# Performance work log

Hardware: AMD Instinct MI355X
Metric: run time of the kernel (lower is better)

The kernel has to match this reference:

```python
import jax, jax.numpy as jnp
import numpy as np

H = 512          # size_half
K = 16           # n_segments
B = 8192         # batch
WIDTH = 1.0 / K  # spline bin width


def setup_inputs() -> dict:
    key = jax.random.key(0)
    ks = jax.random.split(key, 4)
    v_in = jax.random.uniform(ks[0], (B, 2 * H), dtype=jnp.float32)  # config in [0,1]
    log_density = jax.random.normal(ks[1], (B, 1), dtype=jnp.float32)
    W1 = jax.random.normal(ks[2], (H, H), dtype=jnp.float32) * (1.0 / np.sqrt(H))
    b1 = jnp.zeros((H,), dtype=jnp.float32)
    W2 = jax.random.normal(ks[3], (H, H * K), dtype=jnp.float32) * (1.0 / np.sqrt(H))
    b2 = jnp.zeros((H * K,), dtype=jnp.float32)
    return {"v_in": v_in, "log_density": log_density, "W1": W1, "b1": b1, "W2": W2, "b2": b2}


def reference(v_in, log_density, W1, b1, W2, b2):
    # even_sites=True: passive = first half, active = second half
    v_passive = v_in[:, :H]           # [B, H]
    v_active = v_in[:, H:]            # [B, H]

    # FullyConnectedNeuralNetwork: hidden layer + final layer, tanh activation on both
    h = jnp.tanh((v_passive - 0.5) @ W1 + b1)          # [B, H]
    net = jnp.tanh(h @ W2 + b2).reshape(-1, H, K)      # [B, H, K]
    p = jax.nn.softmax(net, axis=2)                    # bin probability masses P_k

    # y-coordinates of knots: CDF of the bin masses, with leading zero
    knots_y = jnp.concatenate(
        [jnp.zeros((p.shape[0], H, 1), p.dtype), jnp.cumsum(p, axis=2)], axis=2
    )                                                  # [B, H, K+1]

    # searchsorted on uniform knots linspace(0,1,K+1), then -1, clamped
    knots_x = jnp.linspace(0.0, 1.0, K + 1, dtype=v_in.dtype)
    k = jnp.clip(jnp.searchsorted(knots_x, v_active, side="left") - 1, 0, K - 1)  # [B, H]

    p_k = jnp.take_along_axis(p, k[..., None], axis=2)[..., 0]        # [B, H]
    y_lo = jnp.take_along_axis(knots_y, k[..., None], axis=2)[..., 0]  # [B, H]

    alpha = (v_active - k.astype(v_in.dtype) * WIDTH) / WIDTH          # [B, H]
    v_out_active = y_lo + alpha * p_k

    v_out = jnp.concatenate([v_passive, v_out_active], axis=1)         # [B, 2H]
    log_density_out = log_density - jnp.sum(jnp.log(p_k), axis=1, keepdims=True)  # [B, 1]
    return v_out, log_density_out
```

## Files before the change

kernel.cpp:

```cpp
#include <hip/hip_runtime.h>
#include <hip/hip_bf16.h>

#define HH   512
#define BB   8192
#define WIDTH (1.0f/16.0f)

typedef __attribute__((ext_vector_type(8))) short  short8;
typedef __attribute__((ext_vector_type(4))) float  floatx4;

typedef const __attribute__((address_space(1))) void* gptr_t;
typedef __attribute__((address_space(3))) void*       lptr_t;

__device__ __forceinline__ void gload_lds16(const void* g, void* l) {
    __builtin_amdgcn_global_load_lds((gptr_t)g, (lptr_t)l, 16, 0, 0);
}

__device__ __forceinline__ float tanh_fast(float x) {
    float e = __expf(2.0f * x);
    return 1.0f - 2.0f * __builtin_amdgcn_rcpf(e + 1.0f);
}

__global__ void prep_all(const float* __restrict__ vin, const float* __restrict__ W1,
                         const float* __restrict__ W2, const float* __restrict__ ld,
                         float* __restrict__ vout, float* __restrict__ ldout,
                         __hip_bfloat16* __restrict__ Abf,
                         __hip_bfloat16* __restrict__ W1T,
                         __hip_bfloat16* __restrict__ W2T) {
    __shared__ __align__(16) float tile[32 * 36];
    int bid = blockIdx.x, tid = threadIdx.x;
    if (bid < 4352) {
        const float* src;  __hip_bfloat16* dst;  int cols, c0, r0;
        if (bid < 4096) { src = W2; dst = W2T; cols = 8192; c0 = (bid & 255) * 32; r0 = (bid >> 8) * 32; }
        else            { int b = bid - 4096; src = W1; dst = W1T; cols = 512; c0 = (b & 15) * 32; r0 = (b >> 4) * 32; }
        int y  = tid >> 3;
        int x0 = (tid & 7) * 4;
        float4 v = *(const float4*)(src + (size_t)(r0 + y) * cols + c0 + x0);
        *(float4*)(tile + y * 36 + x0) = v;
        __syncthreads();
        int n  = tid >> 3;
        int k4 = (tid & 7) * 4;
        union { __hip_bfloat16 h[4]; uint2 u; } o;
        o.h[0] = __float2bfloat16(tile[(k4 + 0) * 36 + n]);
        o.h[1] = __float2bfloat16(tile[(k4 + 1) * 36 + n]);
        o.h[2] = __float2bfloat16(tile[(k4 + 2) * 36 + n]);
        o.h[3] = __float2bfloat16(tile[(k4 + 3) * 36 + n]);
        *(uint2*)(dst + (size_t)(c0 + n) * 512 + r0 + k4) = o.u;
    } else {
        int b = bid - 4352;
        int i = b * 256 + tid;
        int r = i >> 6, c = i & 63;
        const float4* src = (const float4*)(vin + (size_t)r * 1024 + c * 8);
        float4 f0 = src[0], f1 = src[1];
        float4* dst = (float4*)(vout + (size_t)r * 1024 + c * 8);
        dst[0] = f0; dst[1] = f1;
        union { __hip_bfloat16 h[8]; uint4 v; } u;
        u.h[0] = __float2bfloat16(f0.x - 0.5f); u.h[1] = __float2bfloat16(f0.y - 0.5f);
        u.h[2] = __float2bfloat16(f0.z - 0.5f); u.h[3] = __float2bfloat16(f0.w - 0.5f);
        u.h[4] = __float2bfloat16(f1.x - 0.5f); u.h[5] = __float2bfloat16(f1.y - 0.5f);
        u.h[6] = __float2bfloat16(f1.z - 0.5f); u.h[7] = __float2bfloat16(f1.w - 0.5f);
        *(uint4*)(Abf + (size_t)r * 512 + c * 8) = u.v;
        if (tid < 4) { int row = b * 4 + tid; ldout[row] = ld[row]; }
    }
}

__global__ __launch_bounds__(256, 4) void gemm1_kernel(
        const __hip_bfloat16* __restrict__ Abf,
        const __hip_bfloat16* __restrict__ W1T,
        const float* __restrict__ b1,
        __hip_bfloat16* __restrict__ hM) {
    __shared__ __align__(16) char smem[32768];
    short* ldsA = (short*)smem;
    short* ldsB = (short*)(smem + 16384);
    int tid = threadIdx.x;
    int lane = tid & 63;
    int wv = tid >> 6, wr = wv >> 1, wc = wv & 1;
    int q = lane >> 4, cx = lane & 15;
    int srow = tid >> 3;
    int skw  = ((tid & 7) ^ (srow & 7)) * 8;
    int rowBase = blockIdx.y * 128;
    int colBase = blockIdx.x * 128;
    floatx4 acc[4][4] = {};

    for (int k0 = 0; k0 < HH; k0 += 64) {
        #pragma unroll
        for (int j = 0; j < 4; ++j) {
            int row = j * 32 + srow;
            unsigned loff = __builtin_amdgcn_readfirstlane((unsigned)((j * 256 + (tid & 192)) * 16));
            gload_lds16(Abf + (size_t)(rowBase + row) * HH + k0 + skw, (char*)ldsA + loff);
            gload_lds16(W1T + (size_t)(colBase + row) * HH + k0 + skw, (char*)ldsB + loff);
        }
        __syncthreads();
        #pragma unroll
        for (int s = 0; s < 2; ++s) {
            short8 a[4], b[4];
            #pragma unroll
            for (int mt = 0; mt < 4; ++mt)
                a[mt] = *(const short8*)(ldsA + (wr * 64 + mt * 16 + cx) * 64
                                              + (((s * 4 + q) ^ (cx & 7)) << 3));
            #pragma unroll
            for (int nt = 0; nt < 4; ++nt)
                b[nt] = *(const short8*)(ldsB + (wc * 64 + nt * 16 + cx) * 64
                                              + (((s * 4 + q) ^ (cx & 7)) << 3));
            #pragma unroll
            for (int mt = 0; mt < 4; ++mt)
                #pragma unroll
                for (int nt = 0; nt < 4; ++nt)
                    acc[mt][nt] = __builtin_amdgcn_mfma_f32_16x16x32_bf16(a[mt], b[nt], acc[mt][nt], 0, 0, 0);
        }
        __syncthreads();
    }

    float b1v[4];
    #pragma unroll
    for (int nt = 0; nt < 4; ++nt) b1v[nt] = b1[colBase + wc * 64 + nt * 16 + cx];
    #pragma unroll
    for (int mt = 0; mt < 4; ++mt)
        #pragma unroll
        for (int nt = 0; nt < 4; ++nt) {
            int col = colBase + wc * 64 + nt * 16 + cx;
            #pragma unroll
            for (int r = 0; r < 4; ++r) {
                int row = rowBase + wr * 64 + mt * 16 + q * 4 + r;
                hM[(size_t)row * HH + col] = __float2bfloat16(tanh_fast(acc[mt][nt][r] + b1v[nt]));
            }
        }
}

__global__ __launch_bounds__(256, 4) void gemm2_kernel(
        const __hip_bfloat16* __restrict__ hM,
        const __hip_bfloat16* __restrict__ W2T,
        const float* __restrict__ b2,
        const float* __restrict__ vin,
        float* __restrict__ vout,
        float* __restrict__ ldout) {
    __shared__ __align__(16) char smem[32768];
    short* ldsA = (short*)smem;
    short* ldsB = (short*)(smem + 16384);
    float* ldsE = (float*)smem;
    int tid = threadIdx.x;
    int lane = tid & 63;
    int wv = tid >> 6, wr = wv >> 1, wc = wv & 1;
    int q = lane >> 4, cx = lane & 15;
    int srow = tid >> 3;
    int skw  = ((tid & 7) ^ (srow & 7)) * 8;
    int bid = blockIdx.x;
    int xcd = bid & 7, w = bid >> 3;
    int by  = xcd * 8 + (w & 7);
    int bx  = w >> 3;
    int rowBase = by * 128;
    int colBase = bx * 128;
    floatx4 acc[4][4] = {};

    for (int k0 = 0; k0 < HH; k0 += 64) {
        #pragma unroll
        for (int j = 0; j < 4; ++j) {
            int row = j * 32 + srow;
            unsigned loff = __builtin_amdgcn_readfirstlane((unsigned)((j * 256 + (tid & 192)) * 16));
            gload_lds16(hM  + (size_t)(rowBase + row) * HH + k0 + skw, (char*)ldsA + loff);
            gload_lds16(W2T + (size_t)(colBase + row) * HH + k0 + skw, (char*)ldsB + loff);
        }
        __syncthreads();
        #pragma unroll
        for (int s = 0; s < 2; ++s) {
            short8 a[4], b[4];
            #pragma unroll
            for (int mt = 0; mt < 4; ++mt)
                a[mt] = *(const short8*)(ldsA + (wr * 64 + mt * 16 + cx) * 64
                                              + (((s * 4 + q) ^ (cx & 7)) << 3));
            #pragma unroll
            for (int nt = 0; nt < 4; ++nt)
                b[nt] = *(const short8*)(ldsB + (wc * 64 + nt * 16 + cx) * 64
                                              + (((s * 4 + q) ^ (cx & 7)) << 3));
            #pragma unroll
            for (int mt = 0; mt < 4; ++mt)
                #pragma unroll
                for (int nt = 0; nt < 4; ++nt)
                    acc[mt][nt] = __builtin_amdgcn_mfma_f32_16x16x32_bf16(a[mt], b[nt], acc[mt][nt], 0, 0, 0);
        }
        __syncthreads();
    }

    float b2v[4];
    #pragma unroll
    for (int nt = 0; nt < 4; ++nt) b2v[nt] = b2[colBase + wc * 64 + nt * 16 + cx];

    float* myTile = ldsE + wv * (16 * 76);
    int rowL  = lane & 15;
    int gL    = lane >> 4;
    int gAbs  = bx * 8 + wc * 4 + gL;

    #pragma unroll
    for (int mt = 0; mt < 4; ++mt) {
        #pragma unroll
        for (int nt = 0; nt < 4; ++nt)
            #pragma unroll
            for (int r = 0; r < 4; ++r)
                myTile[(q * 4 + r) * 76 + nt * 16 + cx] = acc[mt][nt][r] + b2v[nt];

        floatx4 x0 = *(const floatx4*)(myTile + rowL * 76 + gL * 16);
        floatx4 x1 = *(const floatx4*)(myTile + rowL * 76 + gL * 16 + 4);
        floatx4 x2 = *(const floatx4*)(myTile + rowL * 76 + gL * 16 + 8);
        floatx4 x3 = *(const floatx4*)(myTile + rowL * 76 + gL * 16 + 12);
        float xs[16] = { x0[0],x0[1],x0[2],x0[3], x1[0],x1[1],x1[2],x1[3],
                         x2[0],x2[1],x2[2],x2[3], x3[0],x3[1],x3[2],x3[3] };

        int row = rowBase + wr * 64 + mt * 16 + rowL;
        float v = vin[(size_t)row * 1024 + 512 + gAbs];
        int k = (int)ceilf(v * 16.0f) - 1;
        k = min(15, max(0, k));

        float s = 0.0f, csum = 0.0f, ek = 0.0f;
        #pragma unroll
        for (int j = 0; j < 16; ++j) {
            float e2 = __expf(2.0f * xs[j]);
            float t  = 1.0f - 2.0f * __builtin_amdgcn_rcpf(e2 + 1.0f);
            float e  = __expf(t);
            csum += (j < k)  ? e : 0.0f;
            ek    = (j == k) ? e : ek;
            s += e;
        }
        float rs = __builtin_amdgcn_rcpf(s);
        float pk  = ek * rs;
        float ylo = csum * rs;
        float alpha = (v - (float)k * WIDTH) * 16.0f;
        vout[(size_t)row * 1024 + 512 + gAbs] = ylo + alpha * pk;

        float logp = __logf(pk);
        logp += __shfl_xor(logp, 16, 64);
        logp += __shfl_xor(logp, 32, 64);
        if (lane < 16) atomicAdd(ldout + row, -logp);
    }
}

extern "C" void kernel_launch(void* const* d_in, const int* in_sizes, int n_in,
                              void* d_out, int out_size, void* d_ws, size_t ws_size,
                              hipStream_t stream) {
    const float* vin = (const float*)d_in[0];
    const float* ld  = (const float*)d_in[1];
    const float* W1  = (const float*)d_in[2];
    const float* b1  = (const float*)d_in[3];
    const float* W2  = (const float*)d_in[4];
    const float* b2  = (const float*)d_in[5];
    float* vout  = (float*)d_out;
    float* ldout = vout + (size_t)BB * 1024;

    char* ws = (char*)d_ws;
    __hip_bfloat16* Abf = (__hip_bfloat16*)(ws);
    __hip_bfloat16* W1T = (__hip_bfloat16*)(ws + 8388608);
    __hip_bfloat16* W2T = (__hip_bfloat16*)(ws + 8912896);
    __hip_bfloat16* hM  = (__hip_bfloat16*)(ws + 17301504);

    prep_all<<<6400, 256, 0, stream>>>(vin, W1, W2, ld, vout, ldout, Abf, W1T, W2T);
    gemm1_kernel<<<dim3(4, 64), 256, 0, stream>>>(Abf, W1T, b1, hM);
    gemm2_kernel<<<4096, 256, 0, stream>>>(hM, W2T, b2, vin, vout, ldout);
}
```

Measured before the change: 194.3 us.

## Overlap W2 transpose-convert with first GEMM in a combined kernel

```diff
diff --git a/kernel.cpp b/kernel.cpp
--- a/kernel.cpp
+++ b/kernel.cpp
@@ -20,21 +20,18 @@
     return 1.0f - 2.0f * __builtin_amdgcn_rcpf(e + 1.0f);
 }
 
-__global__ void prep_all(const float* __restrict__ vin, const float* __restrict__ W1,
-                         const float* __restrict__ W2, const float* __restrict__ ld,
-                         float* __restrict__ vout, float* __restrict__ ldout,
-                         __hip_bfloat16* __restrict__ Abf,
-                         __hip_bfloat16* __restrict__ W1T,
-                         __hip_bfloat16* __restrict__ W2T) {
+__global__ void prep_small(const float* __restrict__ vin, const float* __restrict__ W1,
+                           const float* __restrict__ ld,
+                           float* __restrict__ vout, float* __restrict__ ldout,
+                           __hip_bfloat16* __restrict__ Abf,
+                           __hip_bfloat16* __restrict__ W1T) {
     __shared__ __align__(16) float tile[32 * 36];
     int bid = blockIdx.x, tid = threadIdx.x;
-    if (bid < 4352) {
-        const float* src;  __hip_bfloat16* dst;  int cols, c0, r0;
-        if (bid < 4096) { src = W2; dst = W2T; cols = 8192; c0 = (bid & 255) * 32; r0 = (bid >> 8) * 32; }
-        else            { int b = bid - 4096; src = W1; dst = W1T; cols = 512; c0 = (b & 15) * 32; r0 = (b >> 4) * 32; }
+    if (bid < 256) {
+        int c0 = (bid & 15) * 32, r0 = (bid >> 4) * 32;
         int y  = tid >> 3;
         int x0 = (tid & 7) * 4;
-        float4 v = *(const float4*)(src + (size_t)(r0 + y) * cols + c0 + x0);
+        float4 v = *(const float4*)(W1 + (size_t)(r0 + y) * 512 + c0 + x0);
         *(float4*)(tile + y * 36 + x0) = v;
         __syncthreads();
         int n  = tid >> 3;
@@ -44,9 +41,9 @@
         o.h[1] = __float2bfloat16(tile[(k4 + 1) * 36 + n]);
         o.h[2] = __float2bfloat16(tile[(k4 + 2) * 36 + n]);
         o.h[3] = __float2bfloat16(tile[(k4 + 3) * 36 + n]);
-        *(uint2*)(dst + (size_t)(c0 + n) * 512 + r0 + k4) = o.u;
+        *(uint2*)(W1T + (size_t)(c0 + n) * 512 + r0 + k4) = o.u;
     } else {
-        int b = bid - 4352;
+        int b = bid - 256;
         int i = b * 256 + tid;
         int r = i >> 6, c = i & 63;
         const float4* src = (const float4*)(vin + (size_t)r * 1024 + c * 8);
@@ -63,22 +60,43 @@
     }
 }
 
-__global__ __launch_bounds__(256, 4) void gemm1_kernel(
+__global__ __launch_bounds__(256, 4) void mega1_kernel(
         const __hip_bfloat16* __restrict__ Abf,
         const __hip_bfloat16* __restrict__ W1T,
         const float* __restrict__ b1,
-        __hip_bfloat16* __restrict__ hM) {
+        __hip_bfloat16* __restrict__ hM,
+        const float* __restrict__ W2,
+        __hip_bfloat16* __restrict__ W2T) {
     __shared__ __align__(16) char smem[32768];
+    int bid = blockIdx.x, tid = threadIdx.x;
+    if (bid >= 256) {
+        float* tile = (float*)smem;
+        int b = bid - 256;
+        int c0 = (b & 255) * 32, r0 = (b >> 8) * 32;
+        int y  = tid >> 3;
+        int x0 = (tid & 7) * 4;
+        float4 v = *(const float4*)(W2 + (size_t)(r0 + y) * 8192 + c0 + x0);
+        *(float4*)(tile + y * 36 + x0) = v;
+        __syncthreads();
+        int n  = tid >> 3;
+        int k4 = (tid & 7) * 4;
+        union { __hip_bfloat16 h[4]; uint2 u; } o;
+        o.h[0] = __float2bfloat16(tile[(k4 + 0) * 36 + n]);
+        o.h[1] = __float2bfloat16(tile[(k4 + 1) * 36 + n]);
+        o.h[2] = __float2bfloat16(tile[(k4 + 2) * 36 + n]);
+        o.h[3] = __float2bfloat16(tile[(k4 + 3) * 36 + n]);
+        *(uint2*)(W2T + (size_t)(c0 + n) * 512 + r0 + k4) = o.u;
+        return;
+    }
     short* ldsA = (short*)smem;
     short* ldsB = (short*)(smem + 16384);
-    int tid = threadIdx.x;
     int lane = tid & 63;
     int wv = tid >> 6, wr = wv >> 1, wc = wv & 1;
     int q = lane >> 4, cx = lane & 15;
     int srow = tid >> 3;
     int skw  = ((tid & 7) ^ (srow & 7)) * 8;
-    int rowBase = blockIdx.y * 128;
-    int colBase = blockIdx.x * 128;
+    int rowBase = (bid >> 2) * 128;
+    int colBase = (bid & 3) * 128;
     floatx4 acc[4][4] = {};
 
     for (int k0 = 0; k0 < HH; k0 += 64) {
@@ -250,7 +268,7 @@
     __hip_bfloat16* W2T = (__hip_bfloat16*)(ws + 8912896);
     __hip_bfloat16* hM  = (__hip_bfloat16*)(ws + 17301504);
 
-    prep_all<<<6400, 256, 0, stream>>>(vin, W1, W2, ld, vout, ldout, Abf, W1T, W2T);
-    gemm1_kernel<<<dim3(4, 64), 256, 0, stream>>>(Abf, W1T, b1, hM);
+    prep_small<<<2304, 256, 0, stream>>>(vin, W1, ld, vout, ldout, Abf, W1T);
+    mega1_kernel<<<4352, 256, 0, stream>>>(Abf, W1T, b1, hM, W2, W2T);
     gemm2_kernel<<<4096, 256, 0, stream>>>(hM, W2T, b2, vin, vout, ldout);
 }
```

New measurement: 197.0 us. No clear change (+1.4%).

## Fuse prep and both GEMMs into one persistent kernel with grid barriers

Applied to the files above, without the earlier changes.

```diff
diff --git a/kernel.cpp b/kernel.cpp
--- a/kernel.cpp
+++ b/kernel.cpp
@@ -4,6 +4,7 @@
 #define HH   512
 #define BB   8192
 #define WIDTH (1.0f/16.0f)
+#define NBLK 1024u
 
 typedef __attribute__((ext_vector_type(8))) short  short8;
 typedef __attribute__((ext_vector_type(4))) float  floatx4;
@@ -20,215 +21,214 @@
     return 1.0f - 2.0f * __builtin_amdgcn_rcpf(e + 1.0f);
 }
 
-__global__ void prep_all(const float* __restrict__ vin, const float* __restrict__ W1,
-                         const float* __restrict__ W2, const float* __restrict__ ld,
-                         float* __restrict__ vout, float* __restrict__ ldout,
-                         __hip_bfloat16* __restrict__ Abf,
-                         __hip_bfloat16* __restrict__ W1T,
-                         __hip_bfloat16* __restrict__ W2T) {
-    __shared__ __align__(16) float tile[32 * 36];
+__device__ __forceinline__ void grid_barrier(unsigned* cnt) {
+    __syncthreads();
+    if (threadIdx.x == 0) {
+        __threadfence();
+        __hip_atomic_fetch_add(cnt, 1u, __ATOMIC_ACQ_REL, __HIP_MEMORY_SCOPE_AGENT);
+        while (__hip_atomic_load(cnt, __ATOMIC_ACQUIRE, __HIP_MEMORY_SCOPE_AGENT) < NBLK)
+            __builtin_amdgcn_s_sleep(2);
+        __threadfence();
+    }
+    __syncthreads();
+}
+
+__global__ __launch_bounds__(256, 4) void fused_kernel(
+        const float* __restrict__ vin,
+        const float* __restrict__ ld,
+        const float* __restrict__ W1,
+        const float* __restrict__ b1,
+        const float* __restrict__ W2,
+        const float* __restrict__ b2,
+        float* __restrict__ vout,
+        float* __restrict__ ldout,
+        __hip_bfloat16* __restrict__ Abf,
+        __hip_bfloat16* __restrict__ W1T,
+        __hip_bfloat16* __restrict__ W2T,
+        __hip_bfloat16* __restrict__ hM,
+        unsigned* __restrict__ cnt) {
+    __shared__ __align__(16) char smem[32768];
     int bid = blockIdx.x, tid = threadIdx.x;
-    if (bid < 4352) {
-        const float* src;  __hip_bfloat16* dst;  int cols, c0, r0;
-        if (bid < 4096) { src = W2; dst = W2T; cols = 8192; c0 = (bid & 255) * 32; r0 = (bid >> 8) * 32; }
-        else            { int b = bid - 4096; src = W1; dst = W1T; cols = 512; c0 = (b & 15) * 32; r0 = (b >> 4) * 32; }
-        int y  = tid >> 3;
-        int x0 = (tid & 7) * 4;
-        float4 v = *(const float4*)(src + (size_t)(r0 + y) * cols + c0 + x0);
-        *(float4*)(tile + y * 36 + x0) = v;
-        __syncthreads();
-        int n  = tid >> 3;
-        int k4 = (tid & 7) * 4;
-        union { __hip_bfloat16 h[4]; uint2 u; } o;
-        o.h[0] = __float2bfloat16(tile[(k4 + 0) * 36 + n]);
-        o.h[1] = __float2bfloat16(tile[(k4 + 1) * 36 + n]);
-        o.h[2] = __float2bfloat16(tile[(k4 + 2) * 36 + n]);
-        o.h[3] = __float2bfloat16(tile[(k4 + 3) * 36 + n]);
-        *(uint2*)(dst + (size_t)(c0 + n) * 512 + r0 + k4) = o.u;
-    } else {
-        int b = bid - 4352;
-        int i = b * 256 + tid;
-        int r = i >> 6, c = i & 63;
-        const float4* src = (const float4*)(vin + (size_t)r * 1024 + c * 8);
-        float4 f0 = src[0], f1 = src[1];
-        float4* dst = (float4*)(vout + (size_t)r * 1024 + c * 8);
-        dst[0] = f0; dst[1] = f1;
-        union { __hip_bfloat16 h[8]; uint4 v; } u;
-        u.h[0] = __float2bfloat16(f0.x - 0.5f); u.h[1] = __float2bfloat16(f0.y - 0.5f);
-        u.h[2] = __float2bfloat16(f0.z - 0.5f); u.h[3] = __float2bfloat16(f0.w - 0.5f);
-        u.h[4] = __float2bfloat16(f1.x - 0.5f); u.h[5] = __float2bfloat16(f1.y - 0.5f);
-        u.h[6] = __float2bfloat16(f1.z - 0.5f); u.h[7] = __float2bfloat16(f1.w - 0.5f);
-        *(uint4*)(Abf + (size_t)r * 512 + c * 8) = u.v;
-        if (tid < 4) { int row = b * 4 + tid; ldout[row] = ld[row]; }
-    }
-}
-
-__global__ __launch_bounds__(256, 4) void gemm1_kernel(
-        const __hip_bfloat16* __restrict__ Abf,
-        const __hip_bfloat16* __restrict__ W1T,
-        const float* __restrict__ b1,
-        __hip_bfloat16* __restrict__ hM) {
-    __shared__ __align__(16) char smem[32768];
-    short* ldsA = (short*)smem;
-    short* ldsB = (short*)(smem + 16384);
-    int tid = threadIdx.x;
     int lane = tid & 63;
-    int wv = tid >> 6, wr = wv >> 1, wc = wv & 1;
+    int wv = tid >> 6;
     int q = lane >> 4, cx = lane & 15;
     int srow = tid >> 3;
     int skw  = ((tid & 7) ^ (srow & 7)) * 8;
-    int rowBase = blockIdx.y * 128;
-    int colBase = blockIdx.x * 128;
-    floatx4 acc[4][4] = {};
-
-    for (int k0 = 0; k0 < HH; k0 += 64) {
-        #pragma unroll
-        for (int j = 0; j < 4; ++j) {
-            int row = j * 32 + srow;
-            unsigned loff = __builtin_amdgcn_readfirstlane((unsigned)((j * 256 + (tid & 192)) * 16));
-            gload_lds16(Abf + (size_t)(rowBase + row) * HH + k0 + skw, (char*)ldsA + loff);
-            gload_lds16(W1T + (size_t)(colBase + row) * HH + k0 + skw, (char*)ldsB + loff);
-        }
-        __syncthreads();
-        #pragma unroll
-        for (int s = 0; s < 2; ++s) {
-            short8 a[4], b[4];
-            #pragma unroll
-            for (int mt = 0; mt < 4; ++mt)
-                a[mt] = *(const short8*)(ldsA + (wr * 64 + mt * 16 + cx) * 64
-                                              + (((s * 4 + q) ^ (cx & 7)) << 3));
-            #pragma unroll
-            for (int nt = 0; nt < 4; ++nt)
-                b[nt] = *(const short8*)(ldsB + (wc * 64 + nt * 16 + cx) * 64
-                                              + (((s * 4 + q) ^ (cx & 7)) << 3));
-            #pragma unroll
-            for (int mt = 0; mt < 4; ++mt)
-                #pragma unroll
-                for (int nt = 0; nt < 4; ++nt)
-                    acc[mt][nt] = __builtin_amdgcn_mfma_f32_16x16x32_bf16(a[mt], b[nt], acc[mt][nt], 0, 0, 0);
-        }
-        __syncthreads();
-    }
-
-    float b1v[4];
-    #pragma unroll
-    for (int nt = 0; nt < 4; ++nt) b1v[nt] = b1[colBase + wc * 64 + nt * 16 + cx];
-    #pragma unroll
-    for (int mt = 0; mt < 4; ++mt)
+
+    for (int u = bid; u < 4224; u += 1024) {
+        if (u < 2176) {
+            const float* src;  __hip_bfloat16* dst;  int cols, r0, c0;
+            if (u < 2048) { src = W2; dst = W2T; cols = 8192; r0 = (u >> 8) * 64; c0 = (u & 255) * 32; }
+            else { int t = u - 2048; src = W1; dst = W1T; cols = 512; r0 = (t >> 4) * 64; c0 = (t & 15) * 32; }
+            float* tile = (float*)smem;
+            #pragma unroll
+            for (int i = 0; i < 2; ++i) {
+                int c = i * 256 + tid, kr = c >> 3, ng = c & 7;
+                float4 f = *(const float4*)(src + (size_t)(r0 + kr) * cols + c0 + ng * 4);
+                float* tp = tile + kr * 37 + ng * 4;
+                tp[0] = f.x; tp[1] = f.y; tp[2] = f.z; tp[3] = f.w;
+            }
+            __syncthreads();
+            int n = tid >> 3, kc = tid & 7;
+            union { __hip_bfloat16 h[8]; uint4 v; } o;
+            #pragma unroll
+            for (int j = 0; j < 8; ++j)
+                o.h[j] = __float2bfloat16(tile[(kc * 8 + j) * 37 + n]);
+            *(uint4*)(dst + (size_t)(c0 + n) * 512 + r0 + kc * 8) = o.v;
+            __syncthreads();
+        } else {
+            int b = u - 2176;
+            int i = b * 256 + tid;
+            int r = i >> 6, c = i & 63;
+            const float4* src = (const float4*)(vin + (size_t)r * 1024 + c * 8);
+            float4 f0 = src[0], f1 = src[1];
+            float4* dst = (float4*)(vout + (size_t)r * 1024 + c * 8);
+            dst[0] = f0; dst[1] = f1;
+            union { __hip_bfloat16 h[8]; uint4 v; } u8;
+            u8.h[0] = __float2bfloat16(f0.x - 0.5f); u8.h[1] = __float2bfloat16(f0.y - 0.5f);
+            u8.h[2] = __float2bfloat16(f0.z - 0.5f); u8.h[3] = __float2bfloat16(f0.w - 0.5f);
+            u8.h[4] = __float2bfloat16(f1.x - 0.5f); u8.h[5] = __float2bfloat16(f1.y - 0.5f);
+            u8.h[6] = __float2bfloat16(f1.z - 0.5f); u8.h[7] = __float2bfloat16(f1.w - 0.5f);
+            *(uint4*)(Abf + (size_t)r * 512 + c * 8) = u8.v;
+            if (tid < 4) { int row = b * 4 + tid; ldout[row] = ld[row]; }
+        }
+    }
+    grid_barrier(cnt);
+
+    {
+        short* ldsA = (short*)smem;
+        short* ldsB = (short*)(smem + 8192);
+        int rowBase = (bid >> 3) * 64;
+        int colBase = (bid & 7) * 64;
+        floatx4 acc1[4] = {};
+        for (int k0 = 0; k0 < HH; k0 += 64) {
+            #pragma unroll
+            for (int j = 0; j < 2; ++j) {
+                int row = j * 32 + srow;
+                unsigned loff = __builtin_amdgcn_readfirstlane((unsigned)((j * 256 + (tid & 192)) * 16));
+                gload_lds16(Abf + (size_t)(rowBase + row) * HH + k0 + skw, (char*)ldsA + loff);
+                gload_lds16(W1T + (size_t)(colBase + row) * HH + k0 + skw, (char*)ldsB + loff);
+            }
+            __syncthreads();
+            #pragma unroll
+            for (int s = 0; s < 2; ++s) {
+                short8 a = *(const short8*)(ldsA + (wv * 16 + cx) * 64
+                                                 + (((s * 4 + q) ^ (cx & 7)) << 3));
+                #pragma unroll
+                for (int nt = 0; nt < 4; ++nt) {
+                    short8 b = *(const short8*)(ldsB + (nt * 16 + cx) * 64
+                                                     + (((s * 4 + q) ^ (cx & 7)) << 3));
+                    acc1[nt] = __builtin_amdgcn_mfma_f32_16x16x32_bf16(a, b, acc1[nt], 0, 0, 0);
+                }
+            }
+            __syncthreads();
+        }
         #pragma unroll
         for (int nt = 0; nt < 4; ++nt) {
-            int col = colBase + wc * 64 + nt * 16 + cx;
+            int col = colBase + nt * 16 + cx;
+            float bb = b1[col];
             #pragma unroll
             for (int r = 0; r < 4; ++r) {
-                int row = rowBase + wr * 64 + mt * 16 + q * 4 + r;
-                hM[(size_t)row * HH + col] = __float2bfloat16(tanh_fast(acc[mt][nt][r] + b1v[nt]));
-            }
-        }
-}
-
-__global__ __launch_bounds__(256, 4) void gemm2_kernel(
-        const __hip_bfloat16* __restrict__ hM,
-        const __hip_bfloat16* __restrict__ W2T,
-        const float* __restrict__ b2,
-        const float* __restrict__ vin,
-        float* __restrict__ vout,
-        float* __restrict__ ldout) {
-    __shared__ __align__(16) char smem[32768];
+                int row = rowBase + wv * 16 + q * 4 + r;
+                hM[(size_t)row * HH + col] = __float2bfloat16(tanh_fast(acc1[nt][r] + bb));
+            }
+        }
+    }
+    grid_barrier(cnt + 1);
+
     short* ldsA = (short*)smem;
     short* ldsB = (short*)(smem + 16384);
     float* ldsE = (float*)smem;
-    int tid = threadIdx.x;
-    int lane = tid & 63;
-    int wv = tid >> 6, wr = wv >> 1, wc = wv & 1;
-    int q = lane >> 4, cx = lane & 15;
-    int srow = tid >> 3;
-    int skw  = ((tid & 7) ^ (srow & 7)) * 8;
-    int bid = blockIdx.x;
-    int xcd = bid & 7, w = bid >> 3;
-    int by  = xcd * 8 + (w & 7);
-    int bx  = w >> 3;
-    int rowBase = by * 128;
-    int colBase = bx * 128;
-    floatx4 acc[4][4] = {};
-
-    for (int k0 = 0; k0 < HH; k0 += 64) {
+    int wr = wv >> 1, wc = wv & 1;
+    for (int g = 0; g < 4; ++g) {
+        int tt = g * 1024 + bid;
+        int xcd = tt & 7, w = tt >> 3;
+        int by  = xcd * 8 + (w & 7);
+        int bx  = w >> 3;
+        int rowBase = by * 128;
+        int colBase = bx * 128;
+        floatx4 acc[4][4] = {};
+
+        for (int k0 = 0; k0 < HH; k0 += 64) {
+            #pragma unroll
+            for (int j = 0; j < 4; ++j) {
+                int row = j * 32 + srow;
+                unsigned loff = __builtin_amdgcn_readfirstlane((unsigned)((j * 256 + (tid & 192)) * 16));
+                gload_lds16(hM  + (size_t)(rowBase + row) * HH + k0 + skw, (char*)ldsA + loff);
+                gload_lds16(W2T + (size_t)(colBase + row) * HH + k0 + skw, (char*)ldsB + loff);
+            }
+            __syncthreads();
+            #pragma unroll
+            for (int s = 0; s < 2; ++s) {
+                short8 a[4], b[4];
+                #pragma unroll
+                for (int mt = 0; mt < 4; ++mt)
+                    a[mt] = *(const short8*)(ldsA + (wr * 64 + mt * 16 + cx) * 64
+                                                  + (((s * 4 + q) ^ (cx & 7)) << 3));
+                #pragma unroll
+                for (int nt = 0; nt < 4; ++nt)
+                    b[nt] = *(const short8*)(ldsB + (wc * 64 + nt * 16 + cx) * 64
+                                                  + (((s * 4 + q) ^ (cx & 7)) << 3));
+                #pragma unroll
+                for (int mt = 0; mt < 4; ++mt)
+                    #pragma unroll
+                    for (int nt = 0; nt < 4; ++nt)
+                        acc[mt][nt] = __builtin_amdgcn_mfma_f32_16x16x32_bf16(a[mt], b[nt], acc[mt][nt], 0, 0, 0);
+            }
+            __syncthreads();
+        }
+
+        float b2v[4];
         #pragma unroll
-        for (int j = 0; j < 4; ++j) {
-            int row = j * 32 + srow;
-            unsigned loff = __builtin_amdgcn_readfirstlane((unsigned)((j * 256 + (tid & 192)) * 16));
-            gload_lds16(hM  + (size_t)(rowBase + row) * HH + k0 + skw, (char*)ldsA + loff);
-            gload_lds16(W2T + (size_t)(colBase + row) * HH + k0 + skw, (char*)ldsB + loff);
+        for (int nt = 0; nt < 4; ++nt) b2v[nt] = b2[colBase + wc * 64 + nt * 16 + cx];
+
+        float* myTile = ldsE + wv * (16 * 76);
+        int rowL  = lane & 15;
+        int gL    = lane >> 4;
+        int gAbs  = bx * 8 + wc * 4 + gL;
+
+        #pragma unroll
+        for (int mt = 0; mt < 4; ++mt) {
+            #pragma unroll
+            for (int nt = 0; nt < 4; ++nt)
+                #pragma unroll
+                for (int r = 0; r < 4; ++r)
+                    myTile[(q * 4 + r) * 76 + nt * 16 + cx] = acc[mt][nt][r] + b2v[nt];
+
+            floatx4 x0 = *(const floatx4*)(myTile + rowL * 76 + gL * 16);
+            floatx4 x1 = *(const floatx4*)(myTile + rowL * 76 + gL * 16 + 4);
+            floatx4 x2 = *(const floatx4*)(myTile + rowL * 76 + gL * 16 + 8);
+            floatx4 x3 = *(const floatx4*)(myTile + rowL * 76 + gL * 16 + 12);
+            float xs[16] = { x0[0],x0[1],x0[2],x0[3], x1[0],x1[1],x1[2],x1[3],
+                             x2[0],x2[1],x2[2],x2[3], x3[0],x3[1],x3[2],x3[3] };
+
+            int row = rowBase + wr * 64 + mt * 16 + rowL;
+            float v = vin[(size_t)row * 1024 + 512 + gAbs];
+            int k = (int)ceilf(v * 16.0f) - 1;
+            k = min(15, max(0, k));
+
+            float s = 0.0f, csum = 0.0f, ek = 0.0f;
+            #pragma unroll
+            for (int j = 0; j < 16; ++j) {
+                float e2 = __expf(2.0f * xs[j]);
+                float t  = 1.0f - 2.0f * __builtin_amdgcn_rcpf(e2 + 1.0f);
+                float e  = __expf(t);
+                csum += (j < k)  ? e : 0.0f;
+                ek    = (j == k) ? e : ek;
+                s += e;
+            }
+            float rs = __builtin_amdgcn_rcpf(s);
+            float pk  = ek * rs;
+            float ylo = csum * rs;
+            float alpha = (v - (float)k * WIDTH) * 16.0f;
+            vout[(size_t)row * 1024 + 512 + gAbs] = ylo + alpha * pk;
+
+            float logp = __logf(pk);
+            logp += __shfl_xor(logp, 16, 64);
+            logp += __shfl_xor(logp, 32, 64);
+            if (lane < 16) atomicAdd(ldout + row, -logp);
         }
         __syncthreads();
-        #pragma unroll
-        for (int s = 0; s < 2; ++s) {
-            short8 a[4], b[4];
-            #pragma unroll
-            for (int mt = 0; mt < 4; ++mt)
-                a[mt] = *(const short8*)(ldsA + (wr * 64 + mt * 16 + cx) * 64
-                                              + (((s * 4 + q) ^ (cx & 7)) << 3));
-            #pragma unroll
-            for (int nt = 0; nt < 4; ++nt)
-                b[nt] = *(const short8*)(ldsB + (wc * 64 + nt * 16 + cx) * 64
-                                              + (((s * 4 + q) ^ (cx & 7)) << 3));
-            #pragma unroll
-            for (int mt = 0; mt < 4; ++mt)
-                #pragma unroll
-                for (int nt = 0; nt < 4; ++nt)
-                    acc[mt][nt] = __builtin_amdgcn_mfma_f32_16x16x32_bf16(a[mt], b[nt], acc[mt][nt], 0, 0, 0);
-        }
-        __syncthreads();
-    }
-
-    float b2v[4];
-    #pragma unroll
-    for (int nt = 0; nt < 4; ++nt) b2v[nt] = b2[colBase + wc * 64 + nt * 16 + cx];
-
-    float* myTile = ldsE + wv * (16 * 76);
-    int rowL  = lane & 15;
-    int gL    = lane >> 4;
-    int gAbs  = bx * 8 + wc * 4 + gL;
-
-    #pragma unroll
-    for (int mt = 0; mt < 4; ++mt) {
-        #pragma unroll
-        for (int nt = 0; nt < 4; ++nt)
-            #pragma unroll
-            for (int r = 0; r < 4; ++r)
-                myTile[(q * 4 + r) * 76 + nt * 16 + cx] = acc[mt][nt][r] + b2v[nt];
-
-        floatx4 x0 = *(const floatx4*)(myTile + rowL * 76 + gL * 16);
-        floatx4 x1 = *(const floatx4*)(myTile + rowL * 76 + gL * 16 + 4);
-        floatx4 x2 = *(const floatx4*)(myTile + rowL * 76 + gL * 16 + 8);
-        floatx4 x3 = *(const floatx4*)(myTile + rowL * 76 + gL * 16 + 12);
-        float xs[16] = { x0[0],x0[1],x0[2],x0[3], x1[0],x1[1],x1[2],x1[3],
-                         x2[0],x2[1],x2[2],x2[3], x3[0],x3[1],x3[2],x3[3] };
-
-        int row = rowBase + wr * 64 + mt * 16 + rowL;
-        float v = vin[(size_t)row * 1024 + 512 + gAbs];
-        int k = (int)ceilf(v * 16.0f) - 1;
-        k = min(15, max(0, k));
-
-        float s = 0.0f, csum = 0.0f, ek = 0.0f;
-        #pragma unroll
-        for (int j = 0; j < 16; ++j) {
-            float e2 = __expf(2.0f * xs[j]);
-            float t  = 1.0f - 2.0f * __builtin_amdgcn_rcpf(e2 + 1.0f);
-            float e  = __expf(t);
-            csum += (j < k)  ? e : 0.0f;
-            ek    = (j == k) ? e : ek;
-            s += e;
-        }
-        float rs = __builtin_amdgcn_rcpf(s);
-        float pk  = ek * rs;
-        float ylo = csum * rs;
-        float alpha = (v - (float)k * WIDTH) * 16.0f;
-        vout[(size_t)row * 1024 + 512 + gAbs] = ylo + alpha * pk;
-
-        float logp = __logf(pk);
-        logp += __shfl_xor(logp, 16, 64);
-        logp += __shfl_xor(logp, 32, 64);
-        if (lane < 16) atomicAdd(ldout + row, -logp);
     }
 }
 
@@ -249,8 +249,9 @@
     __hip_bfloat16* W1T = (__hip_bfloat16*)(ws + 8388608);
     __hip_bfloat16* W2T = (__hip_bfloat16*)(ws + 8912896);
     __hip_bfloat16* hM  = (__hip_bfloat16*)(ws + 17301504);
-
-    prep_all<<<6400, 256, 0, stream>>>(vin, W1, W2, ld, vout, ldout, Abf, W1T, W2T);
-    gemm1_kernel<<<dim3(4, 64), 256, 0, stream>>>(Abf, W1T, b1, hM);
-    gemm2_kernel<<<4096, 256, 0, stream>>>(hM, W2T, b2, vin, vout, ldout);
-}
+    unsigned* cnt       = (unsigned*)(ws + 25690112);
+
+    hipMemsetAsync(cnt, 0, 8, stream);
+    fused_kernel<<<NBLK, 256, 0, stream>>>(vin, ld, W1, b1, W2, b2,
+                                           vout, ldout, Abf, W1T, W2T, hM, cnt);
+}
```

After: 576.9 us. 2.97x slower.
